# Kernel optimization log

Measured on AMD Instinct MI355X. Metric: run time of the kernel, lower is better.

## Reference

```python
import jax, jax.numpy as jnp
import numpy as np

B, C, T = 16, 512, 1024      # batch, in_shape (channels), seq_len
H, D = 8, 64                 # num_heads, head_dim; embed = H*D == C
E = H * D
EPS = 1e-6


def setup_inputs() -> dict:
    key = jax.random.key(0)
    ks = jax.random.split(key, 10)
    s_in = 1.0 / np.sqrt(C)
    s_e = 1.0 / np.sqrt(E)
    return {
        "X": jax.random.normal(ks[0], (B, C, T), jnp.float32),
        "ln_g": jnp.ones((C,), jnp.float32),
        "ln_b": jnp.zeros((C,), jnp.float32),
        "Wq": jax.random.normal(ks[1], (C, E), jnp.float32) * s_in,
        "bq": jnp.zeros((E,), jnp.float32),
        "Wk": jax.random.normal(ks[2], (C, E), jnp.float32) * s_in,
        "bk": jnp.zeros((E,), jnp.float32),
        "Wv": jax.random.normal(ks[3], (C, E), jnp.float32) * s_in,
        "bv": jnp.zeros((E,), jnp.float32),
        "Wo": jax.random.normal(ks[4], (E, C), jnp.float32) * s_e,
        "bo": jnp.zeros((C,), jnp.float32),
    }


def reference(X, ln_g, ln_b, Wq, bq, Wk, bk, Wv, bv, Wo, bo):
    # dimshuffle: (B, C, T) -> (B, T, C)
    x = jnp.transpose(X, (0, 2, 1))
    # pre-norm LayerNorm over last dim, eps=1e-6
    mu = jnp.mean(x, axis=-1, keepdims=True)
    var = jnp.mean(jnp.square(x - mu), axis=-1, keepdims=True)
    xn = (x - mu) * jax.lax.rsqrt(var + EPS) * ln_g + ln_b
    # QKV projections, split into heads: (B, T, H, D)
    q = (xn @ Wq + bq).reshape(B, T, H, D)
    k = (xn @ Wk + bk).reshape(B, T, H, D)
    v = (xn @ Wv + bv).reshape(B, T, H, D)
    # attention: scores (B, H, T, T)
    scores = jnp.einsum("bqhd,bkhd->bhqk", q, k) / np.sqrt(D)
    w = jax.nn.softmax(scores, axis=-1)
    h = jnp.einsum("bhqk,bkhd->bqhd", w, v).reshape(B, T, E)
    out = h @ Wo + bo            # output projection (dropout=0 in eval)
    out = x + out                # residual
    return jnp.transpose(out, (0, 2, 1))  # back to (B, C, T)
```

## Files before the change

kernel.cpp:

```cpp
#include <hip/hip_runtime.h>
#include <hip/hip_bf16.h>
#include <cstdint>
#include <cstddef>

typedef __attribute__((ext_vector_type(8))) __bf16 bf16x8;
typedef __attribute__((ext_vector_type(4))) float f32x4;
typedef __attribute__((ext_vector_type(16))) float f32x16;
typedef __attribute__((ext_vector_type(4))) unsigned short u16x4;
typedef __attribute__((ext_vector_type(4))) unsigned int u32x4;
typedef unsigned int u32;

#define NB 16
#define NC 512
#define NT 1024
#define NH 8
#define ND 64
#define NE 512

__device__ __forceinline__ void gld16(void* lds, const void* g) {
  __builtin_amdgcn_global_load_lds(
      (const __attribute__((address_space(1))) u32*)g,
      (__attribute__((address_space(3))) u32*)lds, 16, 0, 0);
}

__device__ __forceinline__ unsigned short f2bf(float f) {
  __bf16 h = (__bf16)f;
  return __builtin_bit_cast(unsigned short, h);
}

__device__ __forceinline__ float ex2(float x) {
  float r; asm("v_exp_f32 %0, %1" : "=v"(r) : "v"(x)); return r;
}

__global__ __launch_bounds__(256) void wt_convert4(
    const float* __restrict__ Wq, const float* __restrict__ Wk,
    const float* __restrict__ Wv, const float* __restrict__ Wo,
    __bf16* __restrict__ Wtq, __bf16* __restrict__ Wtk,
    __bf16* __restrict__ Wtv, __bf16* __restrict__ Wto)
{
  __shared__ float tile[32][33];
  const int w = blockIdx.y;
  const float* W = (w == 0) ? Wq : (w == 1) ? Wk : (w == 2) ? Wv : Wo;
  __bf16*     Wt = (w == 0) ? Wtq : (w == 1) ? Wtk : (w == 2) ? Wtv : Wto;
  const int bx = blockIdx.x & 15, by = blockIdx.x >> 4;
  const int r0 = by * 32, c0 = bx * 32;
  const int tx = threadIdx.x & 31, ty = threadIdx.x >> 5;
#pragma unroll
  for (int i = 0; i < 4; i++)
    tile[ty + i * 8][tx] = W[(size_t)(r0 + ty + i * 8) * 512 + c0 + tx];
  __syncthreads();
#pragma unroll
  for (int i = 0; i < 4; i++) {
    const int cc = ty + i * 8;
    Wt[(size_t)(c0 + cc) * 512 + r0 + tx] = (__bf16)tile[tx][cc];
  }
}

__global__ __launch_bounds__(256) void ln_kernel(
    const float* __restrict__ X, const float* __restrict__ gam,
    const float* __restrict__ bet, __bf16* __restrict__ xn)
{
  __shared__ float tile[16][513];
  __shared__ float mu_s[16], rs_s[16];
  const int b  = blockIdx.x >> 6;
  const int t0 = (blockIdx.x & 63) << 4;
  const int tid = threadIdx.x;
  const int tl = tid & 15, c0 = tid >> 4;
  const float* Xb = X + (size_t)b * NC * NT + t0;
  for (int c = c0; c < NC; c += 16)
    tile[tl][c] = Xb[(size_t)c * NT + tl];
  __syncthreads();
  const int row = tid >> 4, sub = tid & 15;
  float s = 0.f, s2 = 0.f;
  for (int c = sub; c < NC; c += 16) { const float v = tile[row][c]; s += v; s2 += v * v; }
  s += __shfl_xor(s, 1);  s2 += __shfl_xor(s2, 1);
  s += __shfl_xor(s, 2);  s2 += __shfl_xor(s2, 2);
  s += __shfl_xor(s, 4);  s2 += __shfl_xor(s2, 4);
  s += __shfl_xor(s, 8);  s2 += __shfl_xor(s2, 8);
  const float mu   = s * (1.f / NC);
  const float var  = s2 * (1.f / NC) - mu * mu;
  const float rstd = rsqrtf(var + 1e-6f);
  if (sub == 0) { mu_s[row] = mu; rs_s[row] = rstd; }
  __syncthreads();
  __bf16* xo = xn + ((size_t)b * NT + t0) * NC;
  for (int i = tid; i < 16 * NC; i += 256) {
    const int r = i >> 9, c = i & (NC - 1);
    xo[(size_t)r * NC + c] = (__bf16)((tile[r][c] - mu_s[r]) * rs_s[r] * gam[c] + bet[c]);
  }
}

__global__ __launch_bounds__(256) void gemm_qkv(
    const __bf16* __restrict__ A, const __bf16* __restrict__ Wt,
    const float* __restrict__ bq, const float* __restrict__ bk, const float* __restrict__ bv,
    __bf16* __restrict__ qb, __bf16* __restrict__ kb, __bf16* __restrict__ vtb)
{
  __shared__ __align__(16) __bf16 lA[128 * 32];
  __shared__ __align__(16) __bf16 lB[128 * 32];
  __shared__ float tb[4][16][17];
  const int tid = threadIdx.x;
  const int wv = tid >> 6, lane = tid & 63;
  const int bid = blockIdx.x;
  const int mchunk = bid / 192, rem = bid % 192;
  const int xcd = rem & 7, loc = rem >> 3;
  const int mt = mchunk * 16 + xcd * 2 + (loc / 12);
  const int nt = loc % 12;
  const int m0 = mt << 7, n0 = nt << 7;
  const int fr = lane & 15, kq = lane >> 4;
  const int wr = wv >> 1, wc = wv & 1;

  const __bf16* Ag0 = A + (size_t)(m0 + (tid >> 2)) * NC + (tid & 3) * 8;
  const __bf16* Ag1 = Ag0 + (size_t)64 * NC;
  const __bf16* Bg0 = Wt + (size_t)(n0 + (tid >> 2)) * NC + (tid & 3) * 8;
  const __bf16* Bg1 = Bg0 + (size_t)64 * NC;
  __bf16* lA0 = lA + wv * 512; __bf16* lA1 = lA + 2048 + wv * 512;
  __bf16* lB0 = lB + wv * 512; __bf16* lB1 = lB + 2048 + wv * 512;

  f32x4 acc[4][4] = {};
  for (int k0 = 0; k0 < NC; k0 += 32) {
    gld16(lA0, Ag0 + k0); gld16(lA1, Ag1 + k0);
    gld16(lB0, Bg0 + k0); gld16(lB1, Bg1 + k0);
    __syncthreads();
    bf16x8 af[4], bfr[4];
#pragma unroll
    for (int i = 0; i < 4; i++) {
      af[i]  = *(const bf16x8*)&lA[(wr * 64 + i * 16 + fr) * 32 + kq * 8];
      bfr[i] = *(const bf16x8*)&lB[(wc * 64 + i * 16 + fr) * 32 + kq * 8];
    }
#pragma unroll
    for (int i = 0; i < 4; i++)
#pragma unroll
      for (int j = 0; j < 4; j++)
        acc[i][j] = __builtin_amdgcn_mfma_f32_16x16x32_bf16(af[i], bfr[j], acc[i][j], 0, 0, 0);
    __syncthreads();
  }

  const int wsel = n0 >> 9;
  const float* bias = (wsel == 0) ? bq : (wsel == 1) ? bk : bv;
  if (wsel < 2) {
#pragma unroll
    for (int i = 0; i < 4; i++) {
#pragma unroll
      for (int j = 0; j < 4; j++) {
        const int ng = (n0 & 511) + wc * 64 + j * 16 + fr;
        const int hh = ng >> 6, dd = ng & 63;
        const float bb = bias[ng];
#pragma unroll
        for (int r = 0; r < 4; r++) {
          const int mg = m0 + wr * 64 + i * 16 + kq * 4 + r;
          const int b = mg >> 10, t = mg & 1023;
          const __bf16 h16 = (__bf16)(acc[i][j][r] + bb);
          if (wsel == 0) qb[(((size_t)b * NH + hh) * NT + t) * ND + dd] = h16;
          else           kb[(((size_t)b * NH + hh) * NT + t) * ND + dd] = h16;
        }
      }
    }
  } else {
#pragma unroll
    for (int i = 0; i < 4; i++) {
#pragma unroll
      for (int j = 0; j < 4; j++) {
#pragma unroll
        for (int r = 0; r < 4; r++) tb[wv][kq * 4 + r][fr] = acc[i][j][r];
#pragma unroll
        for (int rr = 0; rr < 4; rr++) {
          const int cloc = kq * 4 + rr;
          const int ng = (n0 & 511) + wc * 64 + j * 16 + cloc;
          const int hh = ng >> 6, dd = ng & 63;
          const int mg = m0 + wr * 64 + i * 16 + fr;
          const int b = mg >> 10, t = mg & 1023;
          vtb[(((size_t)b * NH + hh) * ND + dd) * NT + t] =
              (__bf16)(tb[wv][fr][cloc] + bias[ng]);
        }
      }
    }
  }
}

__global__ __launch_bounds__(256, 2) void attn_kernel(
    const __bf16* __restrict__ qb, const __bf16* __restrict__ kb,
    const __bf16* __restrict__ vtb, __bf16* __restrict__ hb)
{
  __shared__ __align__(16) __bf16 lK[2][4096];
  __shared__ __align__(16) __bf16 lV[2][4096];
  const int tid = threadIdx.x, wv = tid >> 6, lane = tid & 63;
  const int l31 = lane & 31, hi = lane >> 5;
  const int swz = (l31 & 7) << 4;
  const int bid = blockIdx.x;
  const int xcd = bid & 7, idx = bid >> 3;
  const int hbp = xcd * 16 + (idx >> 2);
  const int chunk = idx & 3;
  const int b = hbp >> 3, hh = hbp & 7;
  const int q0 = chunk * 256 + wv * 64;
  const float C = 0.18033688011112042f;

  const __bf16* Q = qb + ((size_t)b * NH + hh) * NT * ND;
  const char* Kc = (const char*)(kb  + ((size_t)b * NH + hh) * NT * ND);
  const char* Vc = (const char*)(vtb + ((size_t)b * NH + hh) * ND * NT);

  bf16x8 qf[2][4];
#pragma unroll
  for (int qs = 0; qs < 2; qs++)
#pragma unroll
    for (int ds = 0; ds < 4; ds++)
      qf[qs][ds] = *(const bf16x8*)&Q[(size_t)(q0 + qs * 32 + l31) * ND + ds * 16 + hi * 8];

  float m_run[2] = {-3e38f, -3e38f};
  float l_run[2] = {0.f, 0.f};
  f32x16 O[2][2] = {};
  const f32x16 zz = {};

  auto stage = [&](int nb, int kt64) {
#pragma unroll
    for (int is = 0; is < 2; is++) {
      const int o  = is * 4096 + wv * 1024 + lane * 16;
      const int rr = o >> 7;
      const int cb = (o & 127) ^ ((rr & 7) << 4);
      gld16((char*)&lK[nb][0] + is * 4096 + wv * 1024,
            Kc + (size_t)(kt64 + rr) * 128 + cb);
      gld16((char*)&lV[nb][0] + is * 4096 + wv * 1024,
            Vc + (size_t)rr * 2048 + (size_t)kt64 * 2 + cb);
    }
  };

  stage(0, 0);
  __syncthreads();

  for (int ti = 0; ti < 16; ti++) {
    const int cur = ti & 1;
    if (ti < 15) stage(cur ^ 1, (ti + 1) * 64);
    const char* Kb = (const char*)&lK[cur][0];
    const char* Vb = (const char*)&lV[cur][0];

    f32x16 st[2][2];
    __builtin_amdgcn_s_setprio(1);
#pragma unroll
    for (int ks = 0; ks < 2; ks++) {
#pragma unroll
      for (int ds = 0; ds < 4; ds++) {
        const int row = ks * 32 + l31;
        const bf16x8 ka = *(const bf16x8*)
            (Kb + row * 128 + ((ds * 32 + hi * 16) ^ swz));
        if (ds == 0) {
          st[0][ks] = __builtin_amdgcn_mfma_f32_32x32x16_bf16(ka, qf[0][0], zz, 0, 0, 0);
          st[1][ks] = __builtin_amdgcn_mfma_f32_32x32x16_bf16(ka, qf[1][0], zz, 0, 0, 0);
        } else {
          st[0][ks] = __builtin_amdgcn_mfma_f32_32x32x16_bf16(ka, qf[0][ds], st[0][ks], 0, 0, 0);
          st[1][ks] = __builtin_amdgcn_mfma_f32_32x32x16_bf16(ka, qf[1][ds], st[1][ks], 0, 0, 0);
        }
      }
    }
    __builtin_amdgcn_s_setprio(0);

#pragma unroll
    for (int qs = 0; qs < 2; qs++) {
      float tm = -3e38f;
#pragma unroll
      for (int ks = 0; ks < 2; ks++)
#pragma unroll
        for (int r = 0; r < 16; r++) tm = fmaxf(tm, st[qs][ks][r]);
      tm = fmaxf(tm, __shfl_xor(tm, 32));
      const float m_new = fmaxf(m_run[qs], tm * C);
      const float alpha = ex2(m_run[qs] - m_new);
      m_run[qs] = m_new;

      float rs = 0.f;
      u32 pk[2][4][2];
#pragma unroll
      for (int ks = 0; ks < 2; ks++)
#pragma unroll
        for (int g = 0; g < 4; g++) {
          const float p0 = ex2(fmaf(st[qs][ks][4 * g + 0], C, -m_new));
          const float p1 = ex2(fmaf(st[qs][ks][4 * g + 1], C, -m_new));
          const float p2 = ex2(fmaf(st[qs][ks][4 * g + 2], C, -m_new));
          const float p3 = ex2(fmaf(st[qs][ks][4 * g + 3], C, -m_new));
          rs += (p0 + p1) + (p2 + p3);
          asm("v_cvt_pk_bf16_f32 %0, %1, %2" : "=v"(pk[ks][g][0]) : "v"(p0), "v"(p1));
          asm("v_cvt_pk_bf16_f32 %0, %1, %2" : "=v"(pk[ks][g][1]) : "v"(p2), "v"(p3));
        }
      rs += __shfl_xor(rs, 32);
      l_run[qs] = l_run[qs] * alpha + rs;
      O[qs][0] *= alpha;
      O[qs][1] *= alpha;

      __builtin_amdgcn_s_setprio(1);
#pragma unroll
      for (int s = 0; s < 4; s++) {
        const int t = s >> 1, m = s & 1;
        const u32 x0 = hi ? pk[t][2 * m + 1][0] : pk[t][2 * m][0];
        const u32 x1 = hi ? pk[t][2 * m + 1][1] : pk[t][2 * m][1];
        const u32 z0 = hi ? pk[t][2 * m][0]     : pk[t][2 * m + 1][0];
        const u32 z1 = hi ? pk[t][2 * m][1]     : pk[t][2 * m + 1][1];
        const u32 y0 = __shfl_xor(z0, 32);
        const u32 y1 = __shfl_xor(z1, 32);
        u32x4 w;
        w[0] = hi ? y0 : x0;
        w[1] = hi ? y1 : x1;
        w[2] = hi ? x0 : y0;
        w[3] = hi ? x1 : y1;
        const bf16x8 pfrag = __builtin_bit_cast(bf16x8, w);
#pragma unroll
        for (int dsub = 0; dsub < 2; dsub++) {
          const int row = dsub * 32 + l31;
          const bf16x8 vf = *(const bf16x8*)
              (Vb + row * 128 + ((s * 32 + hi * 16) ^ swz));
          O[qs][dsub] = __builtin_amdgcn_mfma_f32_32x32x16_bf16(vf, pfrag, O[qs][dsub], 0, 0, 0);
        }
      }
      __builtin_amdgcn_s_setprio(0);
    }
    __syncthreads();
  }

#pragma unroll
  for (int qs = 0; qs < 2; qs++) {
    const float linv = 1.f / l_run[qs];
    const int t = q0 + qs * 32 + l31;
    __bf16* hrow = hb + ((size_t)b * NT + t) * NE + hh * ND;
#pragma unroll
    for (int dsub = 0; dsub < 2; dsub++)
#pragma unroll
      for (int g = 0; g < 4; g++) {
        u16x4 ov;
#pragma unroll
        for (int rr = 0; rr < 4; rr++) ov[rr] = f2bf(O[qs][dsub][4 * g + rr] * linv);
        *(u16x4*)&hrow[dsub * 32 + g * 8 + hi * 4] = ov;
      }
  }
}

__global__ __launch_bounds__(256) void gemm_out(
    const __bf16* __restrict__ A, const __bf16* __restrict__ Wt,
    const float* __restrict__ bo, const float* __restrict__ X,
    float* __restrict__ out)
{
  __shared__ __align__(16) __bf16 lA[128 * 32];
  __shared__ __align__(16) __bf16 lB[128 * 32];
  __shared__ float tb[4][16][17];
  const int tid = threadIdx.x, wv = tid >> 6, lane = tid & 63;
  const int bid = blockIdx.x;
  const int mt = ((bid >> 5) << 3) + (bid & 7);
  const int nt = (bid & 31) >> 3;
  const int m0 = mt << 7, n0 = nt << 7;
  const int fr = lane & 15, kq = lane >> 4;
  const int wr = wv >> 1, wc = wv & 1;

  const __bf16* Ag0 = A + (size_t)(m0 + (tid >> 2)) * NE + (tid & 3) * 8;
  const __bf16* Ag1 = Ag0 + (size_t)64 * NE;
  const __bf16* Bg0 = Wt + (size_t)(n0 + (tid >> 2)) * NE + (tid & 3) * 8;
  const __bf16* Bg1 = Bg0 + (size_t)64 * NE;
  __bf16* lA0 = lA + wv * 512; __bf16* lA1 = lA + 2048 + wv * 512;
  __bf16* lB0 = lB + wv * 512; __bf16* lB1 = lB + 2048 + wv * 512;

  f32x4 acc[4][4] = {};
  for (int k0 = 0; k0 < NE; k0 += 32) {
    gld16(lA0, Ag0 + k0); gld16(lA1, Ag1 + k0);
    gld16(lB0, Bg0 + k0); gld16(lB1, Bg1 + k0);
    __syncthreads();
    bf16x8 af[4], bfr[4];
#pragma unroll
    for (int i = 0; i < 4; i++) {
      af[i]  = *(const bf16x8*)&lA[(wr * 64 + i * 16 + fr) * 32 + kq * 8];
      bfr[i] = *(const bf16x8*)&lB[(wc * 64 + i * 16 + fr) * 32 + kq * 8];
    }
#pragma unroll
    for (int i = 0; i < 4; i++)
#pragma unroll
      for (int j = 0; j < 4; j++)
        acc[i][j] = __builtin_amdgcn_mfma_f32_16x16x32_bf16(af[i], bfr[j], acc[i][j], 0, 0, 0);
    __syncthreads();
  }

#pragma unroll
  for (int i = 0; i < 4; i++) {
#pragma unroll
    for (int j = 0; j < 4; j++) {
#pragma unroll
      for (int r = 0; r < 4; r++) tb[wv][kq * 4 + r][fr] = acc[i][j][r];
#pragma unroll
      for (int rr = 0; rr < 4; rr++) {
        const int cloc = kq * 4 + rr;
        const int mg = m0 + wr * 64 + i * 16 + fr;
        const int b = mg >> 10, t = mg & 1023;
        const int c = n0 + wc * 64 + j * 16 + cloc;
        out[((size_t)b * NC + c) * NT + t] =
            tb[wv][fr][cloc] + bo[c] + X[((size_t)b * NC + c) * NT + t];
      }
    }
  }
}

extern "C" void kernel_launch(void* const* d_in, const int* in_sizes, int n_in,
                              void* d_out, int out_size, void* d_ws, size_t ws_size,
                              hipStream_t stream) {
  const float* X   = (const float*)d_in[0];
  const float* lng = (const float*)d_in[1];
  const float* lnb = (const float*)d_in[2];
  const float* Wq  = (const float*)d_in[3];
  const float* bq  = (const float*)d_in[4];
  const float* Wk  = (const float*)d_in[5];
  const float* bk  = (const float*)d_in[6];
  const float* Wv  = (const float*)d_in[7];
  const float* bv  = (const float*)d_in[8];
  const float* Wo  = (const float*)d_in[9];
  const float* bo  = (const float*)d_in[10];
  float* out = (float*)d_out;

  __bf16* wsb   = (__bf16*)d_ws;
  __bf16* Wtqkv = wsb;
  __bf16* Wot   = wsb + 786432;
  __bf16* xn    = wsb + 1048576;
  __bf16* qbuf  = wsb + 9437184;
  __bf16* kbuf  = wsb + 17825792;
  __bf16* vtbuf = wsb + 26214400;
  __bf16* hbuf  = wsb + 34603008;

  wt_convert4<<<dim3(256, 4), 256, 0, stream>>>(
      Wq, Wk, Wv, Wo, Wtqkv, Wtqkv + 262144, Wtqkv + 524288, Wot);
  ln_kernel<<<NB * (NT / 16), 256, 0, stream>>>(X, lng, lnb, xn);
  gemm_qkv<<<128 * 12, 256, 0, stream>>>(xn, Wtqkv, bq, bk, bv, qbuf, kbuf, vtbuf);
  attn_kernel<<<512, 256, 0, stream>>>(qbuf, kbuf, vtbuf, hbuf);
  gemm_out<<<128 * 4, 256, 0, stream>>>(hbuf, Wot, bo, X, out);
}
```

Baseline: 154.3 us.

## Fold softmax scale into Q, lazy rescaling, permlane swap, smaller attention blocks

Multiplies Q by the softmax scale (with log2e) in the QKV GEMM epilogue, so the attention kernel computes exp2(s - m) without an extra FMA. It rescales the running max, sum and output only when some lane's new max exceeds the old by more than 8, removing most alpha multiplies. It also replaces the shuffle-based P fragment exchange with v_permlane32_swap, and halves the attention block to 128 threads with twice as many blocks. The lazy rescale lets unnormalised values grow by up to 2^8 before correction, and rounding Q to bf16 after scaling slightly changes numerics.

```diff
diff --git a/kernel.cpp b/kernel.cpp
--- a/kernel.cpp
+++ b/kernel.cpp
@@ -30,6 +30,10 @@
 
 __device__ __forceinline__ float ex2(float x) {
   float r; asm("v_exp_f32 %0, %1" : "=v"(r) : "v"(x)); return r;
+}
+
+__device__ __forceinline__ void pl32swap(u32& a, u32& b) {
+  asm("v_permlane32_swap_b32 %0, %1" : "+v"(a), "+v"(b));
 }
 
 __global__ __launch_bounds__(256) void wt_convert4(
@@ -136,6 +140,7 @@
 
   const int wsel = n0 >> 9;
   const float* bias = (wsel == 0) ? bq : (wsel == 1) ? bk : bv;
+  const float qsc = (wsel == 0) ? 0.18033688011112042f : 1.0f;
   if (wsel < 2) {
 #pragma unroll
     for (int i = 0; i < 4; i++) {
@@ -148,7 +153,7 @@
         for (int r = 0; r < 4; r++) {
           const int mg = m0 + wr * 64 + i * 16 + kq * 4 + r;
           const int b = mg >> 10, t = mg & 1023;
-          const __bf16 h16 = (__bf16)(acc[i][j][r] + bb);
+          const __bf16 h16 = (__bf16)((acc[i][j][r] + bb) * qsc);
           if (wsel == 0) qb[(((size_t)b * NH + hh) * NT + t) * ND + dd] = h16;
           else           kb[(((size_t)b * NH + hh) * NT + t) * ND + dd] = h16;
         }
@@ -176,7 +181,7 @@
   }
 }
 
-__global__ __launch_bounds__(256, 2) void attn_kernel(
+__global__ __launch_bounds__(128, 2) void attn_kernel(
     const __bf16* __restrict__ qb, const __bf16* __restrict__ kb,
     const __bf16* __restrict__ vtb, __bf16* __restrict__ hb)
 {
@@ -187,11 +192,10 @@
   const int swz = (l31 & 7) << 4;
   const int bid = blockIdx.x;
   const int xcd = bid & 7, idx = bid >> 3;
-  const int hbp = xcd * 16 + (idx >> 2);
-  const int chunk = idx & 3;
+  const int hbp = xcd * 16 + (idx >> 3);
+  const int chunk = idx & 7;
   const int b = hbp >> 3, hh = hbp & 7;
-  const int q0 = chunk * 256 + wv * 64;
-  const float C = 0.18033688011112042f;
+  const int q0 = chunk * 128 + wv * 64;
 
   const __bf16* Q = qb + ((size_t)b * NH + hh) * NT * ND;
   const char* Kc = (const char*)(kb  + ((size_t)b * NH + hh) * NT * ND);
@@ -211,13 +215,13 @@
 
   auto stage = [&](int nb, int kt64) {
 #pragma unroll
-    for (int is = 0; is < 2; is++) {
-      const int o  = is * 4096 + wv * 1024 + lane * 16;
+    for (int is = 0; is < 4; is++) {
+      const int o  = is * 2048 + wv * 1024 + lane * 16;
       const int rr = o >> 7;
       const int cb = (o & 127) ^ ((rr & 7) << 4);
-      gld16((char*)&lK[nb][0] + is * 4096 + wv * 1024,
+      gld16((char*)&lK[nb][0] + is * 2048 + wv * 1024,
             Kc + (size_t)(kt64 + rr) * 128 + cb);
-      gld16((char*)&lV[nb][0] + is * 4096 + wv * 1024,
+      gld16((char*)&lV[nb][0] + is * 2048 + wv * 1024,
             Vc + (size_t)rr * 2048 + (size_t)kt64 * 2 + cb);
     }
   };
@@ -259,9 +263,15 @@
 #pragma unroll
         for (int r = 0; r < 16; r++) tm = fmaxf(tm, st[qs][ks][r]);
       tm = fmaxf(tm, __shfl_xor(tm, 32));
-      const float m_new = fmaxf(m_run[qs], tm * C);
-      const float alpha = ex2(m_run[qs] - m_new);
-      m_run[qs] = m_new;
+      if (!__all(tm <= m_run[qs] + 8.f)) {
+        const float m_new = fmaxf(m_run[qs], tm);
+        const float alpha = ex2(m_run[qs] - m_new);
+        m_run[qs] = m_new;
+        l_run[qs] *= alpha;
+        O[qs][0] *= alpha;
+        O[qs][1] *= alpha;
+      }
+      const float mcur = m_run[qs];
 
       float rs = 0.f;
       u32 pk[2][4][2];
@@ -269,34 +279,27 @@
       for (int ks = 0; ks < 2; ks++)
 #pragma unroll
         for (int g = 0; g < 4; g++) {
-          const float p0 = ex2(fmaf(st[qs][ks][4 * g + 0], C, -m_new));
-          const float p1 = ex2(fmaf(st[qs][ks][4 * g + 1], C, -m_new));
-          const float p2 = ex2(fmaf(st[qs][ks][4 * g + 2], C, -m_new));
-          const float p3 = ex2(fmaf(st[qs][ks][4 * g + 3], C, -m_new));
+          const float p0 = ex2(st[qs][ks][4 * g + 0] - mcur);
+          const float p1 = ex2(st[qs][ks][4 * g + 1] - mcur);
+          const float p2 = ex2(st[qs][ks][4 * g + 2] - mcur);
+          const float p3 = ex2(st[qs][ks][4 * g + 3] - mcur);
           rs += (p0 + p1) + (p2 + p3);
           asm("v_cvt_pk_bf16_f32 %0, %1, %2" : "=v"(pk[ks][g][0]) : "v"(p0), "v"(p1));
           asm("v_cvt_pk_bf16_f32 %0, %1, %2" : "=v"(pk[ks][g][1]) : "v"(p2), "v"(p3));
         }
       rs += __shfl_xor(rs, 32);
-      l_run[qs] = l_run[qs] * alpha + rs;
-      O[qs][0] *= alpha;
-      O[qs][1] *= alpha;
+      l_run[qs] += rs;
 
       __builtin_amdgcn_s_setprio(1);
 #pragma unroll
       for (int s = 0; s < 4; s++) {
         const int t = s >> 1, m = s & 1;
-        const u32 x0 = hi ? pk[t][2 * m + 1][0] : pk[t][2 * m][0];
-        const u32 x1 = hi ? pk[t][2 * m + 1][1] : pk[t][2 * m][1];
-        const u32 z0 = hi ? pk[t][2 * m][0]     : pk[t][2 * m + 1][0];
-        const u32 z1 = hi ? pk[t][2 * m][1]     : pk[t][2 * m + 1][1];
-        const u32 y0 = __shfl_xor(z0, 32);
-        const u32 y1 = __shfl_xor(z1, 32);
+        u32 a0 = pk[t][2 * m][0], b0 = pk[t][2 * m + 1][0];
+        u32 a1 = pk[t][2 * m][1], b1 = pk[t][2 * m + 1][1];
+        pl32swap(a0, b0);
+        pl32swap(a1, b1);
         u32x4 w;
-        w[0] = hi ? y0 : x0;
-        w[1] = hi ? y1 : x1;
-        w[2] = hi ? x0 : y0;
-        w[3] = hi ? x1 : y1;
+        w[0] = a0; w[1] = a1; w[2] = b0; w[3] = b1;
         const bf16x8 pfrag = __builtin_bit_cast(bf16x8, w);
 #pragma unroll
         for (int dsub = 0; dsub < 2; dsub++) {
@@ -418,6 +421,6 @@
       Wq, Wk, Wv, Wo, Wtqkv, Wtqkv + 262144, Wtqkv + 524288, Wot);
   ln_kernel<<<NB * (NT / 16), 256, 0, stream>>>(X, lng, lnb, xn);
   gemm_qkv<<<128 * 12, 256, 0, stream>>>(xn, Wtqkv, bq, bk, bv, qbuf, kbuf, vtbuf);
-  attn_kernel<<<512, 256, 0, stream>>>(qbuf, kbuf, vtbuf, hbuf);
+  attn_kernel<<<1024, 128, 0, stream>>>(qbuf, kbuf, vtbuf, hbuf);
   gemm_out<<<128 * 4, 256, 0, stream>>>(hbuf, Wot, bo, X, out);
 }
```

Result: faster. 149.9 us (-2.8%).
